# Optimization experiments

Hardware: AMD Instinct MI355X
Metric: run time of the kernel (lower is better)

## Reference

```python
import jax, jax.numpy as jnp
from jax import lax
import numpy as np


def _rnn_tanh_layer(x, W_ih, W_hh, b_ih, b_hh, return_seq):
    # x: [B, T, I]; W_ih: [H, I]; W_hh: [H, H]
    B = x.shape[0]
    H = W_hh.shape[0]
    # Precompute input projection for all timesteps (one big GEMM).
    xw = jnp.einsum('bti,hi->bth', x, W_ih) + b_ih + b_hh  # [B, T, H]
    xw_t = jnp.swapaxes(xw, 0, 1)  # [T, B, H] for scan
    h0 = jnp.zeros((B, H), dtype=x.dtype)

    def step(h, xt):
        h_new = jnp.tanh(xt + h @ W_hh.T)
        return h_new, (h_new if return_seq else None)

    hT, hs = lax.scan(step, h0, xw_t)
    if return_seq:
        return jnp.swapaxes(hs, 0, 1), hT  # [B, T, H], [B, H]
    return None, hT


def setup_inputs() -> dict:
    key = jax.random.key(0)
    ks = jax.random.split(key, 12)
    B, T, I, H1, H2, C = 512, 1024, 32, 128, 64, 10

    def unif(k, shape, fan):
        bound = 1.0 / np.sqrt(fan)
        return jax.random.uniform(k, shape, jnp.float32, -bound, bound)

    return {
        'x': jax.random.normal(ks[0], (B, T, I), jnp.float32),
        'W_ih1': unif(ks[1], (H1, I), H1),
        'W_hh1': unif(ks[2], (H1, H1), H1),
        'b_ih1': unif(ks[3], (H1,), H1),
        'b_hh1': unif(ks[4], (H1,), H1),
        'W_ih2': unif(ks[5], (H2, H1), H2),
        'W_hh2': unif(ks[6], (H2, H2), H2),
        'b_ih2': unif(ks[7], (H2,), H2),
        'b_hh2': unif(ks[8], (H2,), H2),
        'W_fc': unif(ks[9], (C, H2), H2),
        'b_fc': unif(ks[10], (C,), H2),
    }


def reference(x, W_ih1, W_hh1, b_ih1, b_hh1, W_ih2, W_hh2, b_ih2, b_hh2, W_fc, b_fc):
    out1, _h1 = _rnn_tanh_layer(x, W_ih1, W_hh1, b_ih1, b_hh1, return_seq=True)
    _none, h2 = _rnn_tanh_layer(out1, W_ih2, W_hh2, b_ih2, b_hh2, return_seq=False)
    # Dropout(p=0.3) is identity in eval mode.
    logits = h2 @ W_fc.T + b_fc  # [B, 10]
    return logits
```

## Files before the change

kernel.cpp:

```cpp
#include <hip/hip_runtime.h>
#include <stdint.h>


typedef _Float16 f16x8 __attribute__((ext_vector_type(8)));
typedef float f32x4 __attribute__((ext_vector_type(4)));

#define MFMA_F16(A, B, C) __builtin_amdgcn_mfma_f32_16x16x32_f16((A), (B), (C), 0, 0, 0)

__device__ __forceinline__ float tanh_fast(float x) {
  float t = __builtin_amdgcn_exp2f(x * 2.88539008177792681472f);
  return 1.0f - 2.0f * __builtin_amdgcn_rcpf(t + 1.0f);
}

__device__ __forceinline__ uint32_t pk16(float a, float b) {
  return __builtin_bit_cast(uint32_t, __builtin_amdgcn_cvt_pkrtz(a, b));
}

__device__ __forceinline__ void sync_lds() {
  asm volatile("s_waitcnt lgkmcnt(0)\n\ts_barrier" ::: "memory");
}

__global__ __launch_bounds__(512) void rnn_fused(
    const float* __restrict__ x,
    const float* __restrict__ Wih1, const float* __restrict__ Whh1,
    const float* __restrict__ bih1, const float* __restrict__ bhh1,
    const float* __restrict__ Wih2, const float* __restrict__ Whh2,
    const float* __restrict__ bih2, const float* __restrict__ bhh2,
    const float* __restrict__ Wfc,  const float* __restrict__ bfc,
    float* __restrict__ out)
{
  constexpr int T = 1024, I = 32, H1 = 128, H2 = 64, BB = 16;
  constexpr int R1 = 272, R2 = 144;
  constexpr int H1_0 = 0, H1_1 = 4352;
  constexpr int H2_0 = 8704, H2_1 = 11008;
  constexpr int H2F  = 13312;
  __shared__ __align__(16) unsigned char smem[17408];

  const int tid  = threadIdx.x;
  const int w    = tid >> 6;
  const int lane = tid & 63;
  const int g    = lane >> 4;
  const int n    = lane & 15;
  const int b0   = blockIdx.x * BB;

  {
    uint32_t* p = (uint32_t*)smem;
    for (int i = tid; i < 1088; i += 512) p[i] = 0u;
    uint32_t* q = (uint32_t*)(smem + H2_0);
    for (int i = tid; i < 576; i += 512) q[i] = 0u;
  }

  auto cvt8 = [](const float* s) -> f16x8 {
    f32x4 a = *(const f32x4*)s;
    f32x4 b = *(const f32x4*)(s + 4);
    f16x8 r;
#pragma unroll
    for (int j = 0; j < 4; ++j) { r[j] = (_Float16)a[j]; r[4 + j] = (_Float16)b[j]; }
    return r;
  };

  int roff1[4];
#pragma unroll
  for (int k4 = 0; k4 < 4; ++k4)
    roff1[k4] = n * R1 + k4 * 64 + g * 16;

  auto tanh_pack = [&](const f32x4& a, uint32_t& lo, uint32_t& hi) {
    lo = pk16(tanh_fast(a[0]), tanh_fast(a[1]));
    hi = pk16(tanh_fast(a[2]), tanh_fast(a[3]));
  };

  __syncthreads();

  const f32x4 zero = {0.f, 0.f, 0.f, 0.f};

  if (w < 4) {
    f16x8 aU[2][4], aI1[2];
    f32x4 bias1[2];
#pragma unroll
    for (int ti = 0; ti < 2; ++ti) {
      const int ch = (2 * w + ti) * 16 + n;
#pragma unroll
      for (int k4 = 0; k4 < 4; ++k4)
        aU[ti][k4] = cvt8(Whh1 + ch * H1 + k4 * 32 + g * 8);
      aI1[ti] = cvt8(Wih1 + ch * I + g * 8);
      const int cb = (2 * w + ti) * 16 + g * 4;
#pragma unroll
      for (int r = 0; r < 4; ++r) bias1[ti][r] = bih1[cb + r] + bhh1[cb + r];
    }
    int woff[2];
#pragma unroll
    for (int ti = 0; ti < 2; ++ti)
      woff[ti] = n * R1 + (2 * w + ti) * 32 + g * 8;

    const float* xp = x + (size_t)(b0 + n) * T * I + g * 8;
    f32x4 q0a = *(const f32x4*)(xp + 0 * I), q0b = *(const f32x4*)(xp + 0 * I + 4);
    f32x4 q1a = *(const f32x4*)(xp + 1 * I), q1b = *(const f32x4*)(xp + 1 * I + 4);
    f32x4 q2a = *(const f32x4*)(xp + 2 * I), q2b = *(const f32x4*)(xp + 2 * I + 4);
    f32x4 q3a = *(const f32x4*)(xp + 3 * I), q3b = *(const f32x4*)(xp + 3 * I + 4);

    auto pack_x = [&](const f32x4& a, const f32x4& b) -> f16x8 {
      union { uint32_t u[4]; f16x8 v; } tmp;
      tmp.u[0] = pk16(a[0], a[1]); tmp.u[1] = pk16(a[2], a[3]);
      tmp.u[2] = pk16(b[0], b[1]); tmp.u[3] = pk16(b[2], b[3]);
      return tmp.v;
    };

    f32x4 accI0, accI1;
    {
      f16x8 xf = pack_x(q0a, q0b);
      accI0 = MFMA_F16(aI1[0], xf, bias1[0]);
      accI1 = MFMA_F16(aI1[1], xf, bias1[1]);
    }

    auto stepL1 = [&](int t, int cur, f32x4& la, f32x4& lb,
                      const f32x4& pa, const f32x4& pb) {
      const char* H1c = (const char*)smem + (cur ? H1_1 : H1_0);
      char*       H1n = (char*)smem + (cur ? H1_0 : H1_1);
      f16x8 b1k0 = *(const f16x8*)(H1c + roff1[0]);
      f16x8 b1k1 = *(const f16x8*)(H1c + roff1[1]);
      f16x8 b1k2 = *(const f16x8*)(H1c + roff1[2]);
      f16x8 b1k3 = *(const f16x8*)(H1c + roff1[3]);
      if (t + 4 < T) {
        la = *(const f32x4*)(xp + (t + 4) * I);
        lb = *(const f32x4*)(xp + (t + 4) * I + 4);
      }
      f32x4 aA0 = MFMA_F16(aU[0][0], b1k0, accI0);
      f32x4 aB0 = MFMA_F16(aU[0][2], b1k2, zero);
      f32x4 aA1 = MFMA_F16(aU[1][0], b1k0, accI1);
      f32x4 aB1 = MFMA_F16(aU[1][2], b1k2, zero);
      aA0 = MFMA_F16(aU[0][1], b1k1, aA0);
      aB0 = MFMA_F16(aU[0][3], b1k3, aB0);
      aA1 = MFMA_F16(aU[1][1], b1k1, aA1);
      aB1 = MFMA_F16(aU[1][3], b1k3, aB1);
      {
        f16x8 xf = pack_x(pa, pb);
        accI0 = MFMA_F16(aI1[0], xf, bias1[0]);
        accI1 = MFMA_F16(aI1[1], xf, bias1[1]);
      }
      {
        f32x4 s0 = aA0 + aB0;
        uint32_t lo, hi;
        tanh_pack(s0, lo, hi);
        *(uint2*)(H1n + woff[0]) = make_uint2(lo, hi);
      }
      {
        f32x4 s1 = aA1 + aB1;
        uint32_t lo, hi;
        tanh_pack(s1, lo, hi);
        *(uint2*)(H1n + woff[1]) = make_uint2(lo, hi);
      }
      sync_lds();
    };

    for (int t = 0; t < T; t += 4) {
      stepL1(t + 0, 0, q0a, q0b, q1a, q1b);
      stepL1(t + 1, 1, q1a, q1b, q2a, q2b);
      stepL1(t + 2, 0, q2a, q2b, q3a, q3b);
      stepL1(t + 3, 1, q3a, q3b, q0a, q0b);
    }
  } else {
    const int j = w - 4;
    f16x8 aI2[4], aR2[2];
#pragma unroll
    for (int k4 = 0; k4 < 4; ++k4)
      aI2[k4] = cvt8(Wih2 + (16 * j + n) * H1 + k4 * 32 + g * 8);
#pragma unroll
    for (int k2 = 0; k2 < 2; ++k2)
      aR2[k2] = cvt8(Whh2 + (16 * j + n) * H2 + k2 * 32 + g * 8);
    f32x4 bias2;
#pragma unroll
    for (int r = 0; r < 4; ++r) bias2[r] = bih2[16 * j + g * 4 + r] + bhh2[16 * j + g * 4 + r];

    int roff2[2];
#pragma unroll
    for (int k2 = 0; k2 < 2; ++k2)
      roff2[k2] = n * R2 + k2 * 64 + g * 16;
    const int woff2 = n * R2 + j * 32 + g * 8;

    auto l2_body = [&](const char* H1c, const char* H2r, f32x4& s) {
      f16x8 b1k0 = *(const f16x8*)(H1c + roff1[0]);
      f16x8 b1k1 = *(const f16x8*)(H1c + roff1[1]);
      f16x8 b1k2 = *(const f16x8*)(H1c + roff1[2]);
      f16x8 b1k3 = *(const f16x8*)(H1c + roff1[3]);
      f16x8 b2k0 = *(const f16x8*)(H2r + roff2[0]);
      f16x8 b2k1 = *(const f16x8*)(H2r + roff2[1]);
      f32x4 cA = MFMA_F16(aI2[0], b1k0, bias2);
      f32x4 cB = MFMA_F16(aI2[1], b1k1, zero);
      f32x4 cC = MFMA_F16(aR2[0], b2k0, zero);
      cA = MFMA_F16(aI2[2], b1k2, cA);
      cB = MFMA_F16(aI2[3], b1k3, cB);
      cC = MFMA_F16(aR2[1], b2k1, cC);
      s = cA + cB + cC;
    };

    auto stepL2 = [&](int t, int cur) {
      if (t > 0) {
        const char* H1c = (const char*)smem + (cur ? H1_1 : H1_0);
        const char* H2r = (const char*)smem + (cur ? H2_0 : H2_1);
        char*       H2w = (char*)smem + (cur ? H2_1 : H2_0);
        f32x4 s;
        l2_body(H1c, H2r, s);
        uint32_t lo, hi;
        tanh_pack(s, lo, hi);
        *(uint2*)(H2w + woff2) = make_uint2(lo, hi);
      }
      sync_lds();
    };

    for (int t = 0; t < T; t += 2) {
      stepL2(t + 0, 0);
      stepL2(t + 1, 1);
    }

    {
      f32x4 s;
      l2_body((const char*)smem + H1_0, (const char*)smem + H2_1, s);
      f32x4 hv;
#pragma unroll
      for (int r = 0; r < 4; ++r) hv[r] = tanh_fast(s[r]);
      *(f32x4*)(smem + H2F + n * 256 + (16 * j + 4 * g) * 4) = hv;
    }
  }

  sync_lds();

  if (tid < BB * 10) {
    const int b = tid / 10, c = tid % 10;
    const float* hrow = (const float*)(smem + H2F + b * 256);
    float acc = bfc[c];
#pragma unroll 8
    for (int k = 0; k < 64; ++k) acc += hrow[k] * Wfc[c * 64 + k];
    out[(size_t)(b0 + b) * 10 + c] = acc;
  }
}

extern "C" void kernel_launch(void* const* d_in, const int* in_sizes, int n_in,
                              void* d_out, int out_size, void* d_ws, size_t ws_size,
                              hipStream_t stream) {
  const float* x    = (const float*)d_in[0];
  const float* Wih1 = (const float*)d_in[1];
  const float* Whh1 = (const float*)d_in[2];
  const float* bih1 = (const float*)d_in[3];
  const float* bhh1 = (const float*)d_in[4];
  const float* Wih2 = (const float*)d_in[5];
  const float* Whh2 = (const float*)d_in[6];
  const float* bih2 = (const float*)d_in[7];
  const float* bhh2 = (const float*)d_in[8];
  const float* Wfc  = (const float*)d_in[9];
  const float* bfc  = (const float*)d_in[10];

  hipLaunchKernelGGL(rnn_fused, dim3(512 / 16), dim3(512), 0, stream,
                     x, Wih1, Whh1, bih1, bhh1, Wih2, Whh2, bih2, bhh2,
                     Wfc, bfc, (float*)d_out);
}
```

Measured before the change: 471.7 us.

## Move layer-2 input projection onto layer-1 waves with split-barrier handoff

Layer-1 waves now also compute the layer-2 input projection (Wih2·h1) from the h1 fragments they already load, and write the partial sums to a new LDS buffer. Layer-2 waves then only do the recurrent Whh2 MFMAs plus tanh on their own state. Each step now has two barriers instead of one, which shortens the layer-2 critical path and rebalances MFMA work between the wave groups. An extra trailing step drains the pipeline, and a waves_per_eu(2,2) attribute is added. The cost is more barriers per timestep and more register pressure in the layer-1 waves.

```diff
diff --git a/kernel.cpp b/kernel.cpp
--- a/kernel.cpp
+++ b/kernel.cpp
@@ -20,7 +20,8 @@
   asm volatile("s_waitcnt lgkmcnt(0)\n\ts_barrier" ::: "memory");
 }
 
-__global__ __launch_bounds__(512) void rnn_fused(
+__global__ __attribute__((amdgpu_waves_per_eu(2, 2))) __launch_bounds__(512)
+void rnn_fused(
     const float* __restrict__ x,
     const float* __restrict__ Wih1, const float* __restrict__ Whh1,
     const float* __restrict__ bih1, const float* __restrict__ bhh1,
@@ -31,10 +32,12 @@
 {
   constexpr int T = 1024, I = 32, H1 = 128, H2 = 64, BB = 16;
   constexpr int R1 = 272, R2 = 144;
-  constexpr int H1_0 = 0, H1_1 = 4352;
-  constexpr int H2_0 = 8704, H2_1 = 11008;
-  constexpr int H2F  = 13312;
-  __shared__ __align__(16) unsigned char smem[17408];
+  constexpr int H1_0 = 0;
+  constexpr int H1_1 = 4352;
+  constexpr int H2B  = 8704;
+  constexpr int P2B  = 11008;
+  constexpr int H2F  = 15104;
+  __shared__ __align__(16) unsigned char smem[19200];
 
   const int tid  = threadIdx.x;
   const int w    = tid >> 6;
@@ -46,8 +49,6 @@
   {
     uint32_t* p = (uint32_t*)smem;
     for (int i = tid; i < 1088; i += 512) p[i] = 0u;
-    uint32_t* q = (uint32_t*)(smem + H2_0);
-    for (int i = tid; i < 576; i += 512) q[i] = 0u;
   }
 
   auto cvt8 = [](const float* s) -> f16x8 {
@@ -64,6 +65,8 @@
   for (int k4 = 0; k4 < 4; ++k4)
     roff1[k4] = n * R1 + k4 * 64 + g * 16;
 
+  const int poff = (w & 3) * 1024 + (g * 16 + n) * 16;
+
   auto tanh_pack = [&](const f32x4& a, uint32_t& lo, uint32_t& hi) {
     lo = pk16(tanh_fast(a[0]), tanh_fast(a[1]));
     hi = pk16(tanh_fast(a[2]), tanh_fast(a[3]));
@@ -74,8 +77,8 @@
   const f32x4 zero = {0.f, 0.f, 0.f, 0.f};
 
   if (w < 4) {
-    f16x8 aU[2][4], aI1[2];
-    f32x4 bias1[2];
+    f16x8 aU[2][4], aI1[2], aI2[4];
+    f32x4 bias1[2], bias2v;
 #pragma unroll
     for (int ti = 0; ti < 2; ++ti) {
       const int ch = (2 * w + ti) * 16 + n;
@@ -87,6 +90,13 @@
 #pragma unroll
       for (int r = 0; r < 4; ++r) bias1[ti][r] = bih1[cb + r] + bhh1[cb + r];
     }
+#pragma unroll
+    for (int k4 = 0; k4 < 4; ++k4)
+      aI2[k4] = cvt8(Wih2 + (16 * w + n) * H1 + k4 * 32 + g * 8);
+#pragma unroll
+    for (int r = 0; r < 4; ++r)
+      bias2v[r] = bih2[16 * w + g * 4 + r] + bhh2[16 * w + g * 4 + r];
+
     int woff[2];
 #pragma unroll
     for (int ti = 0; ti < 2; ++ti)
@@ -124,6 +134,10 @@
         la = *(const f32x4*)(xp + (t + 4) * I);
         lb = *(const f32x4*)(xp + (t + 4) * I + 4);
       }
+      f32x4 pA = MFMA_F16(aI2[0], b1k0, bias2v);
+      f32x4 pB = MFMA_F16(aI2[1], b1k1, zero);
+      pA = MFMA_F16(aI2[2], b1k2, pA);
+      pB = MFMA_F16(aI2[3], b1k3, pB);
       f32x4 aA0 = MFMA_F16(aU[0][0], b1k0, accI0);
       f32x4 aB0 = MFMA_F16(aU[0][2], b1k2, zero);
       f32x4 aA1 = MFMA_F16(aU[1][0], b1k0, accI1);
@@ -132,11 +146,9 @@
       aB0 = MFMA_F16(aU[0][3], b1k3, aB0);
       aA1 = MFMA_F16(aU[1][1], b1k1, aA1);
       aB1 = MFMA_F16(aU[1][3], b1k3, aB1);
-      {
-        f16x8 xf = pack_x(pa, pb);
-        accI0 = MFMA_F16(aI1[0], xf, bias1[0]);
-        accI1 = MFMA_F16(aI1[1], xf, bias1[1]);
-      }
+      f32x4 part = pA + pB;
+      *(f32x4*)((char*)smem + P2B + poff) = part;
+      sync_lds();
       {
         f32x4 s0 = aA0 + aB0;
         uint32_t lo, hi;
@@ -148,6 +160,11 @@
         uint32_t lo, hi;
         tanh_pack(s1, lo, hi);
         *(uint2*)(H1n + woff[1]) = make_uint2(lo, hi);
+      }
+      {
+        f16x8 xf = pack_x(pa, pb);
+        accI0 = MFMA_F16(aI1[0], xf, bias1[0]);
+        accI1 = MFMA_F16(aI1[1], xf, bias1[1]);
       }
       sync_lds();
     };
@@ -158,66 +175,54 @@
       stepL1(t + 2, 0, q2a, q2b, q3a, q3b);
       stepL1(t + 3, 1, q3a, q3b, q0a, q0b);
     }
+    stepL1(T, 0, q0a, q0b, q1a, q1b);
   } else {
     const int j = w - 4;
-    f16x8 aI2[4], aR2[2];
-#pragma unroll
-    for (int k4 = 0; k4 < 4; ++k4)
-      aI2[k4] = cvt8(Wih2 + (16 * j + n) * H1 + k4 * 32 + g * 8);
+    f16x8 aR2[2];
 #pragma unroll
     for (int k2 = 0; k2 < 2; ++k2)
       aR2[k2] = cvt8(Whh2 + (16 * j + n) * H2 + k2 * 32 + g * 8);
-    f32x4 bias2;
-#pragma unroll
-    for (int r = 0; r < 4; ++r) bias2[r] = bih2[16 * j + g * 4 + r] + bhh2[16 * j + g * 4 + r];
 
     int roff2[2];
 #pragma unroll
     for (int k2 = 0; k2 < 2; ++k2)
       roff2[k2] = n * R2 + k2 * 64 + g * 16;
     const int woff2 = n * R2 + j * 32 + g * 8;
-
-    auto l2_body = [&](const char* H1c, const char* H2r, f32x4& s) {
-      f16x8 b1k0 = *(const f16x8*)(H1c + roff1[0]);
-      f16x8 b1k1 = *(const f16x8*)(H1c + roff1[1]);
-      f16x8 b1k2 = *(const f16x8*)(H1c + roff1[2]);
-      f16x8 b1k3 = *(const f16x8*)(H1c + roff1[3]);
-      f16x8 b2k0 = *(const f16x8*)(H2r + roff2[0]);
-      f16x8 b2k1 = *(const f16x8*)(H2r + roff2[1]);
-      f32x4 cA = MFMA_F16(aI2[0], b1k0, bias2);
-      f32x4 cB = MFMA_F16(aI2[1], b1k1, zero);
-      f32x4 cC = MFMA_F16(aR2[0], b2k0, zero);
-      cA = MFMA_F16(aI2[2], b1k2, cA);
-      cB = MFMA_F16(aI2[3], b1k3, cB);
-      cC = MFMA_F16(aR2[1], b2k1, cC);
-      s = cA + cB + cC;
+    const int poffr = j * 1024 + (g * 16 + n) * 16;
+
+    f32x4 z2 = zero;
+
+    auto stepL2 = [&](int t) {
+      {
+        uint32_t lo, hi;
+        tanh_pack(z2, lo, hi);
+        *(uint2*)((char*)smem + H2B + woff2) = make_uint2(lo, hi);
+      }
+      sync_lds();
+      if (t > 0) {
+        f32x4 part = *(const f32x4*)((char*)smem + P2B + poffr);
+        f16x8 b2k0 = *(const f16x8*)((char*)smem + H2B + roff2[0]);
+        f16x8 b2k1 = *(const f16x8*)((char*)smem + H2B + roff2[1]);
+        z2 = MFMA_F16(aR2[0], b2k0, part);
+        z2 = MFMA_F16(aR2[1], b2k1, z2);
+      } else {
+        z2 = zero;
+      }
+      sync_lds();
     };
 
-    auto stepL2 = [&](int t, int cur) {
-      if (t > 0) {
-        const char* H1c = (const char*)smem + (cur ? H1_1 : H1_0);
-        const char* H2r = (const char*)smem + (cur ? H2_0 : H2_1);
-        char*       H2w = (char*)smem + (cur ? H2_1 : H2_0);
-        f32x4 s;
-        l2_body(H1c, H2r, s);
-        uint32_t lo, hi;
-        tanh_pack(s, lo, hi);
-        *(uint2*)(H2w + woff2) = make_uint2(lo, hi);
-      }
-      sync_lds();
-    };
-
-    for (int t = 0; t < T; t += 2) {
-      stepL2(t + 0, 0);
-      stepL2(t + 1, 1);
-    }
+    for (int t = 0; t < T; t += 4) {
+      stepL2(t + 0);
+      stepL2(t + 1);
+      stepL2(t + 2);
+      stepL2(t + 3);
+    }
+    stepL2(T);
 
     {
-      f32x4 s;
-      l2_body((const char*)smem + H1_0, (const char*)smem + H2_1, s);
       f32x4 hv;
 #pragma unroll
-      for (int r = 0; r < 4; ++r) hv[r] = tanh_fast(s[r]);
+      for (int r = 0; r < 4; ++r) hv[r] = tanh_fast(z2[r]);
       *(f32x4*)(smem + H2F + n * 256 + (16 * j + 4 * g) * 4) = hv;
     }
   }
```

Result: slower. 499.1 us (+5.8%).

## Precompute layer-1 input projection in a separate parallel kernel

Applied to the files above, without the earlier changes.

Adds a pre-pass kernel that computes x·W_ih1 + biases for every timestep, spread across 256 blocks, and writes the result as fp16 into the workspace in the MFMA accumulator layout. The recurrent kernel then loads these precomputed values instead of converting x and running input MFMAs on the serial per-step critical path. The catch is an extra launch and roughly 128 MB of workspace write and read traffic, plus fp16 rounding of the projection. The original path is kept as a fallback when the workspace is too small.

```diff
diff --git a/kernel.cpp b/kernel.cpp
--- a/kernel.cpp
+++ b/kernel.cpp
@@ -3,6 +3,7 @@
 
 
 typedef _Float16 f16x8 __attribute__((ext_vector_type(8)));
+typedef _Float16 f16x4 __attribute__((ext_vector_type(4)));
 typedef float f32x4 __attribute__((ext_vector_type(4)));
 
 #define MFMA_F16(A, B, C) __builtin_amdgcn_mfma_f32_16x16x32_f16((A), (B), (C), 0, 0, 0)
@@ -20,13 +21,74 @@
   asm volatile("s_waitcnt lgkmcnt(0)\n\ts_barrier" ::: "memory");
 }
 
-__global__ __launch_bounds__(512) void rnn_fused(
+__device__ __forceinline__ f16x8 cvt8w(const float* s) {
+  f32x4 a = *(const f32x4*)s;
+  f32x4 b = *(const f32x4*)(s + 4);
+  f16x8 r;
+#pragma unroll
+  for (int j = 0; j < 4; ++j) { r[j] = (_Float16)a[j]; r[4 + j] = (_Float16)b[j]; }
+  return r;
+}
+
+__device__ __forceinline__ f16x8 pack_x8(const f32x4& a, const f32x4& b) {
+  union { uint32_t u[4]; f16x8 v; } tmp;
+  tmp.u[0] = pk16(a[0], a[1]); tmp.u[1] = pk16(a[2], a[3]);
+  tmp.u[2] = pk16(b[0], b[1]); tmp.u[3] = pk16(b[2], b[3]);
+  return tmp.v;
+}
+
+__global__ __launch_bounds__(256) void xw_pre(
+    const float* __restrict__ x, const float* __restrict__ Wih1,
+    const float* __restrict__ bih1, const float* __restrict__ bhh1,
+    uint2* __restrict__ xw)
+{
+  const int tid  = threadIdx.x;
+  const int w    = tid >> 6, lane = tid & 63;
+  const int g    = lane >> 4, n = lane & 15;
+  const int gb   = blockIdx.x >> 3;
+  const int t0   = ((blockIdx.x & 7) << 7) + (w << 5);
+
+  f16x8 aI[8];
+  f32x4 bias[8];
+#pragma unroll
+  for (int m = 0; m < 8; ++m) {
+    aI[m] = cvt8w(Wih1 + (m * 16 + n) * 32 + g * 8);
+#pragma unroll
+    for (int r = 0; r < 4; ++r)
+      bias[m][r] = bih1[m * 16 + g * 4 + r] + bhh1[m * 16 + g * 4 + r];
+  }
+
+  const float* xp = x + ((size_t)(gb * 16 + n) * 1024 + t0) * 32 + g * 8;
+  uint2* xo = xw + (size_t)(gb * 1024 + t0) * 512 + lane;
+
+  f32x4 xa = *(const f32x4*)(xp);
+  f32x4 xb = *(const f32x4*)(xp + 4);
+  for (int tt = 0; tt < 32; ++tt) {
+    f32x4 na, nb;
+    if (tt < 31) {
+      na = *(const f32x4*)(xp + (tt + 1) * 32);
+      nb = *(const f32x4*)(xp + (tt + 1) * 32 + 4);
+    }
+    f16x8 xf = pack_x8(xa, xb);
+#pragma unroll
+    for (int m = 0; m < 8; ++m) {
+      f32x4 d = MFMA_F16(aI[m], xf, bias[m]);
+      xo[tt * 512 + m * 64] = make_uint2(pk16(d[0], d[1]), pk16(d[2], d[3]));
+    }
+    xa = na; xb = nb;
+  }
+}
+
+template <bool USE_XW>
+__global__ __attribute__((amdgpu_waves_per_eu(2, 2))) __launch_bounds__(512)
+void rnn_rec(
     const float* __restrict__ x,
     const float* __restrict__ Wih1, const float* __restrict__ Whh1,
     const float* __restrict__ bih1, const float* __restrict__ bhh1,
     const float* __restrict__ Wih2, const float* __restrict__ Whh2,
     const float* __restrict__ bih2, const float* __restrict__ bhh2,
     const float* __restrict__ Wfc,  const float* __restrict__ bfc,
+    const uint2* __restrict__ xw,
     float* __restrict__ out)
 {
   constexpr int T = 1024, I = 32, H1 = 128, H2 = 64, BB = 16;
@@ -50,15 +112,6 @@
     for (int i = tid; i < 576; i += 512) q[i] = 0u;
   }
 
-  auto cvt8 = [](const float* s) -> f16x8 {
-    f32x4 a = *(const f32x4*)s;
-    f32x4 b = *(const f32x4*)(s + 4);
-    f16x8 r;
-#pragma unroll
-    for (int j = 0; j < 4; ++j) { r[j] = (_Float16)a[j]; r[4 + j] = (_Float16)b[j]; }
-    return r;
-  };
-
   int roff1[4];
 #pragma unroll
   for (int k4 = 0; k4 < 4; ++k4)
@@ -74,99 +127,153 @@
   const f32x4 zero = {0.f, 0.f, 0.f, 0.f};
 
   if (w < 4) {
-    f16x8 aU[2][4], aI1[2];
-    f32x4 bias1[2];
+    f16x8 aU[2][4];
 #pragma unroll
     for (int ti = 0; ti < 2; ++ti) {
       const int ch = (2 * w + ti) * 16 + n;
 #pragma unroll
       for (int k4 = 0; k4 < 4; ++k4)
-        aU[ti][k4] = cvt8(Whh1 + ch * H1 + k4 * 32 + g * 8);
-      aI1[ti] = cvt8(Wih1 + ch * I + g * 8);
-      const int cb = (2 * w + ti) * 16 + g * 4;
-#pragma unroll
-      for (int r = 0; r < 4; ++r) bias1[ti][r] = bih1[cb + r] + bhh1[cb + r];
+        aU[ti][k4] = cvt8w(Whh1 + ch * H1 + k4 * 32 + g * 8);
     }
     int woff[2];
 #pragma unroll
     for (int ti = 0; ti < 2; ++ti)
       woff[ti] = n * R1 + (2 * w + ti) * 32 + g * 8;
 
-    const float* xp = x + (size_t)(b0 + n) * T * I + g * 8;
-    f32x4 q0a = *(const f32x4*)(xp + 0 * I), q0b = *(const f32x4*)(xp + 0 * I + 4);
-    f32x4 q1a = *(const f32x4*)(xp + 1 * I), q1b = *(const f32x4*)(xp + 1 * I + 4);
-    f32x4 q2a = *(const f32x4*)(xp + 2 * I), q2b = *(const f32x4*)(xp + 2 * I + 4);
-    f32x4 q3a = *(const f32x4*)(xp + 3 * I), q3b = *(const f32x4*)(xp + 3 * I + 4);
-
-    auto pack_x = [&](const f32x4& a, const f32x4& b) -> f16x8 {
-      union { uint32_t u[4]; f16x8 v; } tmp;
-      tmp.u[0] = pk16(a[0], a[1]); tmp.u[1] = pk16(a[2], a[3]);
-      tmp.u[2] = pk16(b[0], b[1]); tmp.u[3] = pk16(b[2], b[3]);
-      return tmp.v;
-    };
-
-    f32x4 accI0, accI1;
-    {
-      f16x8 xf = pack_x(q0a, q0b);
-      accI0 = MFMA_F16(aI1[0], xf, bias1[0]);
-      accI1 = MFMA_F16(aI1[1], xf, bias1[1]);
-    }
-
-    auto stepL1 = [&](int t, int cur, f32x4& la, f32x4& lb,
-                      const f32x4& pa, const f32x4& pb) {
-      const char* H1c = (const char*)smem + (cur ? H1_1 : H1_0);
-      char*       H1n = (char*)smem + (cur ? H1_0 : H1_1);
-      f16x8 b1k0 = *(const f16x8*)(H1c + roff1[0]);
-      f16x8 b1k1 = *(const f16x8*)(H1c + roff1[1]);
-      f16x8 b1k2 = *(const f16x8*)(H1c + roff1[2]);
-      f16x8 b1k3 = *(const f16x8*)(H1c + roff1[3]);
-      if (t + 4 < T) {
-        la = *(const f32x4*)(xp + (t + 4) * I);
-        lb = *(const f32x4*)(xp + (t + 4) * I + 4);
-      }
-      f32x4 aA0 = MFMA_F16(aU[0][0], b1k0, accI0);
-      f32x4 aB0 = MFMA_F16(aU[0][2], b1k2, zero);
-      f32x4 aA1 = MFMA_F16(aU[1][0], b1k0, accI1);
-      f32x4 aB1 = MFMA_F16(aU[1][2], b1k2, zero);
-      aA0 = MFMA_F16(aU[0][1], b1k1, aA0);
-      aB0 = MFMA_F16(aU[0][3], b1k3, aB0);
-      aA1 = MFMA_F16(aU[1][1], b1k1, aA1);
-      aB1 = MFMA_F16(aU[1][3], b1k3, aB1);
+    if constexpr (USE_XW) {
+      const uint2* xwp = xw + (size_t)blockIdx.x * T * 512 + lane;
+      const int ti0 = (2 * w) * 64, ti1 = (2 * w + 1) * 64;
+
+      auto cvtC = [](uint2 v) -> f32x4 {
+        f16x4 h = __builtin_bit_cast(f16x4, v);
+        f32x4 r;
+#pragma unroll
+        for (int i = 0; i < 4; ++i) r[i] = (float)h[i];
+        return r;
+      };
+
+      uint2 qA0 = xwp[0 * 512 + ti0], qA1 = xwp[0 * 512 + ti1];
+      uint2 qB0 = xwp[1 * 512 + ti0], qB1 = xwp[1 * 512 + ti1];
+
+      auto stepL1 = [&](int t, int cur, uint2& s0, uint2& s1) {
+        const char* H1c = (const char*)smem + (cur ? H1_1 : H1_0);
+        char*       H1n = (char*)smem + (cur ? H1_0 : H1_1);
+        f16x8 b1k0 = *(const f16x8*)(H1c + roff1[0]);
+        f16x8 b1k1 = *(const f16x8*)(H1c + roff1[1]);
+        f16x8 b1k2 = *(const f16x8*)(H1c + roff1[2]);
+        f16x8 b1k3 = *(const f16x8*)(H1c + roff1[3]);
+        f32x4 accI0 = cvtC(s0), accI1 = cvtC(s1);
+        if (t + 2 < T) {
+          s0 = xwp[(t + 2) * 512 + ti0];
+          s1 = xwp[(t + 2) * 512 + ti1];
+        }
+        f32x4 aA0 = MFMA_F16(aU[0][0], b1k0, accI0);
+        f32x4 aB0 = MFMA_F16(aU[0][2], b1k2, zero);
+        f32x4 aA1 = MFMA_F16(aU[1][0], b1k0, accI1);
+        f32x4 aB1 = MFMA_F16(aU[1][2], b1k2, zero);
+        aA0 = MFMA_F16(aU[0][1], b1k1, aA0);
+        aB0 = MFMA_F16(aU[0][3], b1k3, aB0);
+        aA1 = MFMA_F16(aU[1][1], b1k1, aA1);
+        aB1 = MFMA_F16(aU[1][3], b1k3, aB1);
+        {
+          f32x4 s0v = aA0 + aB0;
+          uint32_t lo, hi;
+          tanh_pack(s0v, lo, hi);
+          *(uint2*)(H1n + woff[0]) = make_uint2(lo, hi);
+        }
+        {
+          f32x4 s1v = aA1 + aB1;
+          uint32_t lo, hi;
+          tanh_pack(s1v, lo, hi);
+          *(uint2*)(H1n + woff[1]) = make_uint2(lo, hi);
+        }
+        sync_lds();
+      };
+
+      for (int t = 0; t < T; t += 2) {
+        stepL1(t + 0, 0, qA0, qA1);
+        stepL1(t + 1, 1, qB0, qB1);
+      }
+    } else {
+      f16x8 aI1[2];
+      f32x4 bias1[2];
+#pragma unroll
+      for (int ti = 0; ti < 2; ++ti) {
+        const int ch = (2 * w + ti) * 16 + n;
+        aI1[ti] = cvt8w(Wih1 + ch * I + g * 8);
+        const int cb = (2 * w + ti) * 16 + g * 4;
+#pragma unroll
+        for (int r = 0; r < 4; ++r) bias1[ti][r] = bih1[cb + r] + bhh1[cb + r];
+      }
+      const float* xp = x + (size_t)(b0 + n) * T * I + g * 8;
+      f32x4 q0a = *(const f32x4*)(xp + 0 * I), q0b = *(const f32x4*)(xp + 0 * I + 4);
+      f32x4 q1a = *(const f32x4*)(xp + 1 * I), q1b = *(const f32x4*)(xp + 1 * I + 4);
+      f32x4 q2a = *(const f32x4*)(xp + 2 * I), q2b = *(const f32x4*)(xp + 2 * I + 4);
+      f32x4 q3a = *(const f32x4*)(xp + 3 * I), q3b = *(const f32x4*)(xp + 3 * I + 4);
+
+      f32x4 accI0, accI1;
       {
-        f16x8 xf = pack_x(pa, pb);
+        f16x8 xf = pack_x8(q0a, q0b);
         accI0 = MFMA_F16(aI1[0], xf, bias1[0]);
         accI1 = MFMA_F16(aI1[1], xf, bias1[1]);
       }
-      {
-        f32x4 s0 = aA0 + aB0;
-        uint32_t lo, hi;
-        tanh_pack(s0, lo, hi);
-        *(uint2*)(H1n + woff[0]) = make_uint2(lo, hi);
-      }
-      {
-        f32x4 s1 = aA1 + aB1;
-        uint32_t lo, hi;
-        tanh_pack(s1, lo, hi);
-        *(uint2*)(H1n + woff[1]) = make_uint2(lo, hi);
-      }
-      sync_lds();
-    };
-
-    for (int t = 0; t < T; t += 4) {
-      stepL1(t + 0, 0, q0a, q0b, q1a, q1b);
-      stepL1(t + 1, 1, q1a, q1b, q2a, q2b);
-      stepL1(t + 2, 0, q2a, q2b, q3a, q3b);
-      stepL1(t + 3, 1, q3a, q3b, q0a, q0b);
+
+      auto stepL1 = [&](int t, int cur, f32x4& la, f32x4& lb,
+                        const f32x4& pa, const f32x4& pb) {
+        const char* H1c = (const char*)smem + (cur ? H1_1 : H1_0);
+        char*       H1n = (char*)smem + (cur ? H1_0 : H1_1);
+        f16x8 b1k0 = *(const f16x8*)(H1c + roff1[0]);
+        f16x8 b1k1 = *(const f16x8*)(H1c + roff1[1]);
+        f16x8 b1k2 = *(const f16x8*)(H1c + roff1[2]);
+        f16x8 b1k3 = *(const f16x8*)(H1c + roff1[3]);
+        if (t + 4 < T) {
+          la = *(const f32x4*)(xp + (t + 4) * I);
+          lb = *(const f32x4*)(xp + (t + 4) * I + 4);
+        }
+        f32x4 aA0 = MFMA_F16(aU[0][0], b1k0, accI0);
+        f32x4 aB0 = MFMA_F16(aU[0][2], b1k2, zero);
+        f32x4 aA1 = MFMA_F16(aU[1][0], b1k0, accI1);
+        f32x4 aB1 = MFMA_F16(aU[1][2], b1k2, zero);
+        aA0 = MFMA_F16(aU[0][1], b1k1, aA0);
+        aB0 = MFMA_F16(aU[0][3], b1k3, aB0);
+        aA1 = MFMA_F16(aU[1][1], b1k1, aA1);
+        aB1 = MFMA_F16(aU[1][3], b1k3, aB1);
+        {
+          f16x8 xf = pack_x8(pa, pb);
+          accI0 = MFMA_F16(aI1[0], xf, bias1[0]);
+          accI1 = MFMA_F16(aI1[1], xf, bias1[1]);
+        }
+        {
+          f32x4 s0 = aA0 + aB0;
+          uint32_t lo, hi;
+          tanh_pack(s0, lo, hi);
+          *(uint2*)(H1n + woff[0]) = make_uint2(lo, hi);
+        }
+        {
+          f32x4 s1 = aA1 + aB1;
+          uint32_t lo, hi;
+          tanh_pack(s1, lo, hi);
+          *(uint2*)(H1n + woff[1]) = make_uint2(lo, hi);
+        }
+        sync_lds();
+      };
+
+      for (int t = 0; t < T; t += 4) {
+        stepL1(t + 0, 0, q0a, q0b, q1a, q1b);
+        stepL1(t + 1, 1, q1a, q1b, q2a, q2b);
+        stepL1(t + 2, 0, q2a, q2b, q3a, q3b);
+        stepL1(t + 3, 1, q3a, q3b, q0a, q0b);
+      }
     }
   } else {
     const int j = w - 4;
     f16x8 aI2[4], aR2[2];
 #pragma unroll
     for (int k4 = 0; k4 < 4; ++k4)
-      aI2[k4] = cvt8(Wih2 + (16 * j + n) * H1 + k4 * 32 + g * 8);
+      aI2[k4] = cvt8w(Wih2 + (16 * j + n) * H1 + k4 * 32 + g * 8);
 #pragma unroll
     for (int k2 = 0; k2 < 2; ++k2)
-      aR2[k2] = cvt8(Whh2 + (16 * j + n) * H2 + k2 * 32 + g * 8);
+      aR2[k2] = cvt8w(Whh2 + (16 * j + n) * H2 + k2 * 32 + g * 8);
     f32x4 bias2;
 #pragma unroll
     for (int r = 0; r < 4; ++r) bias2[r] = bih2[16 * j + g * 4 + r] + bhh2[16 * j + g * 4 + r];
@@ -249,7 +356,17 @@
   const float* Wfc  = (const float*)d_in[9];
   const float* bfc  = (const float*)d_in[10];
 
-  hipLaunchKernelGGL(rnn_fused, dim3(512 / 16), dim3(512), 0, stream,
-                     x, Wih1, Whh1, bih1, bhh1, Wih2, Whh2, bih2, bhh2,
-                     Wfc, bfc, (float*)d_out);
-}
+  const size_t xw_bytes = (size_t)512 * 1024 * 128 * 2;
+  if (ws_size >= xw_bytes) {
+    uint2* xw = (uint2*)d_ws;
+    hipLaunchKernelGGL(xw_pre, dim3(256), dim3(256), 0, stream,
+                       x, Wih1, bih1, bhh1, xw);
+    hipLaunchKernelGGL((rnn_rec<true>), dim3(512 / 16), dim3(512), 0, stream,
+                       x, Wih1, Whh1, bih1, bhh1, Wih2, Whh2, bih2, bhh2,
+                       Wfc, bfc, (const uint2*)xw, (float*)d_out);
+  } else {
+    hipLaunchKernelGGL((rnn_rec<false>), dim3(512 / 16), dim3(512), 0, stream,
+                       x, Wih1, Whh1, bih1, bhh1, Wih2, Whh2, bih2, bhh2,
+                       Wfc, bfc, (const uint2*)nullptr, (float*)d_out);
+  }
+}
```

New measurement: 433.1 us. 8.2% less time.
